# Optimization experiments

Hardware: AMD Instinct MI355X
Metric: run time of the kernel (lower is better)

## Reference

```python
import jax, jax.numpy as jnp
import numpy as np

EMBED_DIM = 1024
NUM_HEADS = 16
HEAD_DIM = EMBED_DIM // NUM_HEADS


def setup_inputs() -> dict:
    key = jax.random.key(0)
    ks = jax.random.split(key, 5)
    B, T, C = 2, 2048, EMBED_DIM
    s_in = 1.0 / np.sqrt(C)
    x = jax.random.normal(ks[0], (B, T, C), dtype=jnp.float32)
    W_qkv = jax.random.normal(ks[1], (C, 3 * C), dtype=jnp.float32) * s_in
    b_qkv = jnp.zeros((3 * C,), dtype=jnp.float32)
    W_out = jax.random.normal(ks[2], (C, C), dtype=jnp.float32) * s_in
    b_out = jnp.zeros((C,), dtype=jnp.float32)
    return {"x": x, "W_qkv": W_qkv, "b_qkv": b_qkv, "W_out": W_out, "b_out": b_out}


def reference(x, W_qkv, b_qkv, W_out, b_out):
    B, T, C = x.shape
    H, D = NUM_HEADS, HEAD_DIM
    qkv = x @ W_qkv + b_qkv                      # [B,T,3C]
    qkv = qkv.reshape(B, T, 3, H, D)
    q = jnp.transpose(qkv[:, :, 0], (0, 2, 1, 3))  # [B,H,T,D]
    k = jnp.transpose(qkv[:, :, 1], (0, 2, 1, 3))
    v = jnp.transpose(qkv[:, :, 2], (0, 2, 1, 3))
    scores = jnp.einsum('bhtd,bhsd->bhts', q, k) / np.sqrt(D).astype(jnp.float32)
    attn = jax.nn.softmax(scores, axis=-1)
    ctx = jnp.einsum('bhts,bhsd->bhtd', attn, v)   # [B,H,T,D]
    ctx = jnp.transpose(ctx, (0, 2, 1, 3)).reshape(B, T, C)
    return ctx @ W_out + b_out
```

## Files before the change

kernel.cpp:

```cpp
#include <hip/hip_runtime.h>
#include <hip/hip_bf16.h>


typedef __attribute__((ext_vector_type(8)))  short short8;
typedef __attribute__((ext_vector_type(4)))  float floatx4;
typedef __attribute__((ext_vector_type(16))) float floatx16;

__device__ inline ushort f2bf(float f) {
    union { __hip_bfloat16 h; ushort u; } c; c.h = __float2bfloat16(f); return c.u;
}

__device__ inline void gld16(const ushort* g, ushort* l) {
    __builtin_amdgcn_global_load_lds(
        (__attribute__((address_space(1))) void*)(g),
        (__attribute__((address_space(3))) void*)(l), 16, 0, 0);
}

__device__ inline void tile_transpose(const float* __restrict__ src, ushort* __restrict__ dst,
                                      int R, int C, int rt, int ct, int t, ushort* L)
{
    const int row = t >> 2, cc = (t & 3) * 16;
    const float* sp = src + (long)(rt * 64 + row) * C + ct * 64 + cc;
    ushort tmp[16];
    #pragma unroll
    for (int i = 0; i < 4; i++) {
        float4 v = *(const float4*)(sp + i * 4);
        tmp[i*4+0]=f2bf(v.x); tmp[i*4+1]=f2bf(v.y); tmp[i*4+2]=f2bf(v.z); tmp[i*4+3]=f2bf(v.w);
    }
    *(uint4*)&L[row * 72 + cc]     = *(uint4*)&tmp[0];
    *(uint4*)&L[row * 72 + cc + 8] = *(uint4*)&tmp[8];
    __syncthreads();
    const int c = t >> 2, rc = (t & 3) * 16;
    ushort o[16];
    #pragma unroll
    for (int j = 0; j < 16; j++) o[j] = L[(rc + j) * 72 + c];
    ushort* dp = dst + (long)(ct * 64 + c) * R + rt * 64 + rc;
    *(uint4*)dp       = *(uint4*)&o[0];
    *(uint4*)(dp + 8) = *(uint4*)&o[8];
}

__global__ __launch_bounds__(256) void prep_kernel(
    const float* __restrict__ x, const float* __restrict__ Wqkv, const float* __restrict__ Wout,
    ushort* __restrict__ xb, ushort* __restrict__ wqkvT, ushort* __restrict__ woutT)
{
    __shared__ __align__(16) ushort L[64 * 72];
    const int bid = blockIdx.x, t = threadIdx.x;
    if (bid < 2048) {
        long i = ((long)bid * 256 + t) * 8;
        float4 a = *(const float4*)(x + i);
        float4 b = *(const float4*)(x + i + 4);
        ushort tmp[8] = { f2bf(a.x), f2bf(a.y), f2bf(a.z), f2bf(a.w),
                          f2bf(b.x), f2bf(b.y), f2bf(b.z), f2bf(b.w) };
        *(uint4*)(xb + i) = *(uint4*)tmp;
    } else if (bid < 2048 + 768) {
        int idx = bid - 2048;
        tile_transpose(Wqkv, wqkvT, 1024, 3072, idx & 15, idx >> 4, t, L);
    } else {
        int idx = bid - 2048 - 768;
        tile_transpose(Wout, woutT, 1024, 1024, idx & 15, idx >> 4, t, L);
    }
}

__global__ __launch_bounds__(256) void qkv_gemm_kernel(
    const ushort* __restrict__ A, const ushort* __restrict__ Bt,
    const float* __restrict__ bias,
    ushort* __restrict__ qbuf, ushort* __restrict__ kbuf, ushort* __restrict__ vtmp)
{
    __shared__ __align__(16) ushort As[2][128 * 32];
    __shared__ __align__(16) ushort Bs[2][128 * 32];

    const int t = threadIdx.x;
    const int w = t >> 6, lane = t & 63;
    const int r = lane & 15, qq = lane >> 4;
    const int wm = w >> 1, wn = w & 1;
    const int rowBase = blockIdx.y * 128, colBase = blockIdx.x * 128;

    const int g_row = lane >> 2, g_kc = (lane & 3) * 8;
    const ushort* aP0 = A  + (long)(rowBase +      w * 16 + g_row) * 1024 + g_kc;
    const ushort* aP1 = A  + (long)(rowBase + 64 + w * 16 + g_row) * 1024 + g_kc;
    const ushort* bP0 = Bt + (long)(colBase +      w * 16 + g_row) * 1024 + g_kc;
    const ushort* bP1 = Bt + (long)(colBase + 64 + w * 16 + g_row) * 1024 + g_kc;

    floatx4 acc[4][4] = {};

    for (int k0 = 0; k0 < 1024; k0 += 64) {
        #pragma unroll
        for (int kk = 0; kk < 2; kk++) {
            gld16(aP0 + k0 + kk * 32, &As[kk][(w * 16) * 32]);
            gld16(aP1 + k0 + kk * 32, &As[kk][(64 + w * 16) * 32]);
            gld16(bP0 + k0 + kk * 32, &Bs[kk][(w * 16) * 32]);
            gld16(bP1 + k0 + kk * 32, &Bs[kk][(64 + w * 16) * 32]);
        }
        __syncthreads();
        #pragma unroll
        for (int kk = 0; kk < 2; kk++) {
            short8 af[4], bf4[4];
            #pragma unroll
            for (int tm = 0; tm < 4; tm++) af[tm]  = *(const short8*)&As[kk][(wm * 64 + tm * 16 + r) * 32 + qq * 8];
            #pragma unroll
            for (int tn = 0; tn < 4; tn++) bf4[tn] = *(const short8*)&Bs[kk][(wn * 64 + tn * 16 + r) * 32 + qq * 8];
            #pragma unroll
            for (int tm = 0; tm < 4; tm++)
                #pragma unroll
                for (int tn = 0; tn < 4; tn++)
                    acc[tm][tn] = __builtin_amdgcn_mfma_f32_16x16x32_bf16(af[tm], bf4[tn], acc[tm][tn], 0, 0, 0);
        }
        __syncthreads();
    }

    #pragma unroll
    for (int tn = 0; tn < 4; tn++) {
        int col = colBase + wn * 64 + tn * 16 + r;
        float bvv = bias[col];
        #pragma unroll
        for (int tm = 0; tm < 4; tm++) {
            #pragma unroll
            for (int reg = 0; reg < 4; reg++) {
                int row = rowBase + wm * 64 + tm * 16 + qq * 4 + reg;
                float val = acc[tm][tn][reg] + bvv;
                if (colBase < 1024)       qbuf[(long)row * 1024 + col]        = f2bf(val);
                else if (colBase < 2048)  kbuf[(long)row * 1024 + col - 1024] = f2bf(val);
                else                      vtmp[(long)row * 1024 + col - 2048] = f2bf(val);
            }
        }
    }
}

__global__ __launch_bounds__(256) void vtrans_kernel(
    const ushort* __restrict__ vsrc, ushort* __restrict__ vt)
{
    __shared__ __align__(16) ushort L[64 * 72];
    const int tt = blockIdx.x, bh = blockIdx.y;
    const int b = bh >> 4, h = bh & 15;
    const int t = threadIdx.x;
    const int row = t >> 2, cc = (t & 3) * 16;
    const ushort* src = vsrc + (long)(b * 2048 + tt * 64 + row) * 1024 + h * 64 + cc;
    *(uint4*)&L[row * 72 + cc]     = *(const uint4*)src;
    *(uint4*)&L[row * 72 + cc + 8] = *(const uint4*)(src + 8);
    __syncthreads();
    const int d = t >> 2, tc = (t & 3) * 16;
    ushort tmp[16];
    #pragma unroll
    for (int j = 0; j < 16; j++) tmp[j] = L[(tc + j) * 72 + d];
    ushort* dst = vt + (long)(bh * 64 + d) * 2048 + tt * 64 + tc;
    *(uint4*)dst       = *(uint4*)&tmp[0];
    *(uint4*)(dst + 8) = *(uint4*)&tmp[8];
}

__global__ __launch_bounds__(256) void out_gemm_kernel(
    const ushort* __restrict__ A, const ushort* __restrict__ Bt,
    const float* __restrict__ bias, float* __restrict__ out)
{
    __shared__ __align__(16) ushort As[2][128 * 32];
    __shared__ __align__(16) ushort Bs[2][64 * 32];

    const int t = threadIdx.x;
    const int w = t >> 6, lane = t & 63;
    const int r = lane & 15, qq = lane >> 4;
    const int wm = w >> 1, wn = w & 1;
    const int rowBase = blockIdx.y * 128, colBase = blockIdx.x * 64;

    const int g_row = lane >> 2, g_kc = (lane & 3) * 8;
    const ushort* aP0 = A  + (long)(rowBase +      w * 16 + g_row) * 1024 + g_kc;
    const ushort* aP1 = A  + (long)(rowBase + 64 + w * 16 + g_row) * 1024 + g_kc;
    const ushort* bP0 = Bt + (long)(colBase +      w * 16 + g_row) * 1024 + g_kc;

    floatx4 acc[4][2] = {};

    for (int k0 = 0; k0 < 1024; k0 += 64) {
        #pragma unroll
        for (int kk = 0; kk < 2; kk++) {
            gld16(aP0 + k0 + kk * 32, &As[kk][(w * 16) * 32]);
            gld16(aP1 + k0 + kk * 32, &As[kk][(64 + w * 16) * 32]);
            gld16(bP0 + k0 + kk * 32, &Bs[kk][(w * 16) * 32]);
        }
        __syncthreads();
        #pragma unroll
        for (int kk = 0; kk < 2; kk++) {
            short8 af[4], bf2[2];
            #pragma unroll
            for (int tm = 0; tm < 4; tm++) af[tm]  = *(const short8*)&As[kk][(wm * 64 + tm * 16 + r) * 32 + qq * 8];
            #pragma unroll
            for (int tn = 0; tn < 2; tn++) bf2[tn] = *(const short8*)&Bs[kk][(wn * 32 + tn * 16 + r) * 32 + qq * 8];
            #pragma unroll
            for (int tm = 0; tm < 4; tm++)
                #pragma unroll
                for (int tn = 0; tn < 2; tn++)
                    acc[tm][tn] = __builtin_amdgcn_mfma_f32_16x16x32_bf16(af[tm], bf2[tn], acc[tm][tn], 0, 0, 0);
        }
        __syncthreads();
    }

    #pragma unroll
    for (int tn = 0; tn < 2; tn++) {
        int col = colBase + wn * 32 + tn * 16 + r;
        float bvv = bias[col];
        #pragma unroll
        for (int tm = 0; tm < 4; tm++) {
            #pragma unroll
            for (int reg = 0; reg < 4; reg++) {
                int row = rowBase + wm * 64 + tm * 16 + qq * 4 + reg;
                out[(long)row * 1024 + col] = acc[tm][tn][reg] + bvv;
            }
        }
    }
}

#define CSCALE 0.18033688011112042f
#define MSHIFT 34.62468098133512f

__global__ __launch_bounds__(256) void attn_kernel(
    ushort* __restrict__ qbuf, const ushort* __restrict__ kbuf,
    const ushort* __restrict__ vt)
{
    __shared__ __align__(16) ushort Ks[64 * 72];
    __shared__ __align__(16) ushort Vs[64 * 72];

    const int t = threadIdx.x;
    const int w = t >> 6, lane = t & 63;
    const int m32 = lane & 31, hi = lane >> 5;

    const int qt = blockIdx.x;
    const int bh = blockIdx.y;
    const int b = bh >> 4, h = bh & 15;
    const long qrow = (long)(b * 2048 + qt * 128 + w * 32 + m32);

    short8 qfrag[4];
    #pragma unroll
    for (int dc = 0; dc < 4; dc++)
        qfrag[dc] = *(const short8*)(qbuf + qrow * 1024 + h * 64 + dc * 16 + hi * 8);

    const int srow = t >> 2, scol = (t & 3) * 16;
    const ushort* kbase = kbuf + (long)(b * 2048) * 1024 + h * 64;
    const ushort* vbase = vt + (long)(bh * 64) * 2048;

    floatx16 o[2] = {};
    float lsum = 0.f;

    for (int kt = 0; kt < 32; kt++) {
        __syncthreads();
        {
            const ushort* kp = kbase + (long)(kt * 64 + srow) * 1024 + scol;
            *(uint4*)&Ks[srow * 72 + scol]     = *(const uint4*)kp;
            *(uint4*)&Ks[srow * 72 + scol + 8] = *(const uint4*)(kp + 8);
            const ushort* vp = vbase + (long)srow * 2048 + kt * 64 + scol;
            *(uint4*)&Vs[srow * 72 + scol]     = *(const uint4*)vp;
            *(uint4*)&Vs[srow * 72 + scol + 8] = *(const uint4*)(vp + 8);
        }
        __syncthreads();

        floatx16 s[2] = {};
        #pragma unroll
        for (int c = 0; c < 2; c++) {
            #pragma unroll
            for (int dc = 0; dc < 4; dc++) {
                short8 kf = *(const short8*)&Ks[(c * 32 + m32) * 72 + dc * 16 + hi * 8];
                s[c] = __builtin_amdgcn_mfma_f32_32x32x16_bf16(kf, qfrag[dc], s[c], 0, 0, 0);
            }
        }

        uint pk[2][8];
        #pragma unroll
        for (int c = 0; c < 2; c++) {
            #pragma unroll
            for (int i = 0; i < 8; i++) {
                float p0 = __builtin_amdgcn_exp2f(s[c][2 * i]     * CSCALE - MSHIFT);
                float p1 = __builtin_amdgcn_exp2f(s[c][2 * i + 1] * CSCALE - MSHIFT);
                lsum += p0 + p1;
                pk[c][i] = (uint)f2bf(p0) | ((uint)f2bf(p1) << 16);
            }
        }

        #pragma unroll
        for (int c = 0; c < 2; c++) {
            #pragma unroll
            for (int kc = 0; kc < 2; kc++) {
                uint s0 = hi ? pk[c][4 * kc + 0] : pk[c][4 * kc + 2];
                uint s1 = hi ? pk[c][4 * kc + 1] : pk[c][4 * kc + 3];
                uint r0 = (uint)__shfl_xor((int)s0, 32);
                uint r1 = (uint)__shfl_xor((int)s1, 32);
                union { uint u[4]; short8 s8; } cv;
                cv.u[0] = hi ? r0 : pk[c][4 * kc + 0];
                cv.u[1] = hi ? r1 : pk[c][4 * kc + 1];
                cv.u[2] = hi ? pk[c][4 * kc + 2] : r0;
                cv.u[3] = hi ? pk[c][4 * kc + 3] : r1;
                #pragma unroll
                for (int dt = 0; dt < 2; dt++) {
                    short8 vf = *(const short8*)&Vs[(dt * 32 + m32) * 72 + c * 32 + kc * 16 + hi * 8];
                    o[dt] = __builtin_amdgcn_mfma_f32_32x32x16_bf16(vf, cv.s8, o[dt], 0, 0, 0);
                }
            }
        }
    }

    lsum += __shfl_xor(lsum, 32);
    float inv = 1.f / lsum;

    #pragma unroll
    for (int dt = 0; dt < 2; dt++) {
        #pragma unroll
        for (int g = 0; g < 4; g++) {
            ushort tmp[4] = { f2bf(o[dt][4*g+0] * inv), f2bf(o[dt][4*g+1] * inv),
                              f2bf(o[dt][4*g+2] * inv), f2bf(o[dt][4*g+3] * inv) };
            *(uint2*)(qbuf + qrow * 1024 + h * 64 + dt * 32 + g * 8 + hi * 4) = *(uint2*)tmp;
        }
    }
}

extern "C" void kernel_launch(void* const* d_in, const int* in_sizes, int n_in,
                              void* d_out, int out_size, void* d_ws, size_t ws_size,
                              hipStream_t stream) {
    const float* x     = (const float*)d_in[0];
    const float* W_qkv = (const float*)d_in[1];
    const float* b_qkv = (const float*)d_in[2];
    const float* W_out = (const float*)d_in[3];
    const float* b_out = (const float*)d_in[4];
    float* out = (float*)d_out;

    ushort* qbuf  = (ushort*)d_ws;
    ushort* kbuf  = qbuf + (size_t)4096 * 1024;
    ushort* vt    = kbuf + (size_t)4096 * 1024;
    ushort* wqkvT = vt + (size_t)2048 * 2048;
    ushort* woutT = wqkvT;

    ushort* xb    = (ushort*)d_out;
    ushort* vtmp  = xb + (size_t)4096 * 1024;

    dim3 blk(256);
    ushort* wqkvT2 = woutT + (size_t)1024 * 1024;

    prep_kernel<<<3072, blk, 0, stream>>>(x, W_qkv, W_out, xb, wqkvT2, woutT);
    qkv_gemm_kernel<<<dim3(24, 32), blk, 0, stream>>>(xb, wqkvT2, b_qkv, qbuf, kbuf, vtmp);
    vtrans_kernel<<<dim3(32, 32), blk, 0, stream>>>(vtmp, vt);
    attn_kernel<<<dim3(16, 32), blk, 0, stream>>>(qbuf, kbuf, vt);
    out_gemm_kernel<<<dim3(16, 32), blk, 0, stream>>>(qbuf, woutT, b_out, out);
}
```

Measured before the change: 207.6 us.

## Prefetch K/V tiles into registers, fold softmax scale into Q, cheaper bf16 pack

The attention kernel now loads the next K/V tile into registers during the current tile's compute and only stores to LDS at the start of each iteration. This hides global load latency and removes one barrier wait on memory. The softmax scale is folded into Q in the QKV GEMM epilogue, dropping a multiply per score, and the bf16 conversion of probabilities uses a simple round-half-up bit trick instead of the library conversion. Workspace pointer naming is also cleaned up. The costs are extra registers and slightly different rounding.

After: 204.2 us. Within noise of the previous version (-1.6%).

```diff
diff --git a/kernel.cpp b/kernel.cpp
--- a/kernel.cpp
+++ b/kernel.cpp
@@ -61,6 +61,8 @@
     }
 }
 
+#define QSCALE 0.18033688011112042f
+
 __global__ __launch_bounds__(256) void qkv_gemm_kernel(
     const ushort* __restrict__ A, const ushort* __restrict__ Bt,
     const float* __restrict__ bias,
@@ -118,7 +120,7 @@
             for (int reg = 0; reg < 4; reg++) {
                 int row = rowBase + wm * 64 + tm * 16 + qq * 4 + reg;
                 float val = acc[tm][tn][reg] + bvv;
-                if (colBase < 1024)       qbuf[(long)row * 1024 + col]        = f2bf(val);
+                if (colBase < 1024)       qbuf[(long)row * 1024 + col]        = f2bf(val * QSCALE);
                 else if (colBase < 2048)  kbuf[(long)row * 1024 + col - 1024] = f2bf(val);
                 else                      vtmp[(long)row * 1024 + col - 2048] = f2bf(val);
             }
@@ -206,7 +208,6 @@
     }
 }
 
-#define CSCALE 0.18033688011112042f
 #define MSHIFT 34.62468098133512f
 
 __global__ __launch_bounds__(256) void attn_kernel(
@@ -237,17 +238,28 @@
     floatx16 o[2] = {};
     float lsum = 0.f;
 
+    uint4 kr0, kr1, vr0, vr1;
+    {
+        const ushort* kp = kbase + (long)srow * 1024 + scol;
+        kr0 = *(const uint4*)kp; kr1 = *(const uint4*)(kp + 8);
+        const ushort* vp = vbase + (long)srow * 2048 + scol;
+        vr0 = *(const uint4*)vp; vr1 = *(const uint4*)(vp + 8);
+    }
+
     for (int kt = 0; kt < 32; kt++) {
         __syncthreads();
-        {
-            const ushort* kp = kbase + (long)(kt * 64 + srow) * 1024 + scol;
-            *(uint4*)&Ks[srow * 72 + scol]     = *(const uint4*)kp;
-            *(uint4*)&Ks[srow * 72 + scol + 8] = *(const uint4*)(kp + 8);
-            const ushort* vp = vbase + (long)srow * 2048 + kt * 64 + scol;
-            *(uint4*)&Vs[srow * 72 + scol]     = *(const uint4*)vp;
-            *(uint4*)&Vs[srow * 72 + scol + 8] = *(const uint4*)(vp + 8);
-        }
-        __syncthreads();
+        *(uint4*)&Ks[srow * 72 + scol]     = kr0;
+        *(uint4*)&Ks[srow * 72 + scol + 8] = kr1;
+        *(uint4*)&Vs[srow * 72 + scol]     = vr0;
+        *(uint4*)&Vs[srow * 72 + scol + 8] = vr1;
+        __syncthreads();
+
+        if (kt < 31) {
+            const ushort* kp = kbase + (long)((kt + 1) * 64 + srow) * 1024 + scol;
+            kr0 = *(const uint4*)kp; kr1 = *(const uint4*)(kp + 8);
+            const ushort* vp = vbase + (long)srow * 2048 + (kt + 1) * 64 + scol;
+            vr0 = *(const uint4*)vp; vr1 = *(const uint4*)(vp + 8);
+        }
 
         floatx16 s[2] = {};
         #pragma unroll
@@ -264,10 +276,12 @@
         for (int c = 0; c < 2; c++) {
             #pragma unroll
             for (int i = 0; i < 8; i++) {
-                float p0 = __builtin_amdgcn_exp2f(s[c][2 * i]     * CSCALE - MSHIFT);
-                float p1 = __builtin_amdgcn_exp2f(s[c][2 * i + 1] * CSCALE - MSHIFT);
+                float p0 = __builtin_amdgcn_exp2f(s[c][2 * i]     - MSHIFT);
+                float p1 = __builtin_amdgcn_exp2f(s[c][2 * i + 1] - MSHIFT);
                 lsum += p0 + p1;
-                pk[c][i] = (uint)f2bf(p0) | ((uint)f2bf(p1) << 16);
+                uint ua = __float_as_uint(p0) + 0x8000u;
+                uint ub = __float_as_uint(p1) + 0x8000u;
+                pk[c][i] = (ua >> 16) | (ub & 0xFFFF0000u);
             }
         }
 
@@ -320,17 +334,15 @@
     ushort* qbuf  = (ushort*)d_ws;
     ushort* kbuf  = qbuf + (size_t)4096 * 1024;
     ushort* vt    = kbuf + (size_t)4096 * 1024;
-    ushort* wqkvT = vt + (size_t)2048 * 2048;
-    ushort* woutT = wqkvT;
+    ushort* woutT = vt + (size_t)2048 * 2048;
+    ushort* wqkvT = woutT + (size_t)1024 * 1024;
 
     ushort* xb    = (ushort*)d_out;
     ushort* vtmp  = xb + (size_t)4096 * 1024;
 
     dim3 blk(256);
-    ushort* wqkvT2 = woutT + (size_t)1024 * 1024;
-
-    prep_kernel<<<3072, blk, 0, stream>>>(x, W_qkv, W_out, xb, wqkvT2, woutT);
-    qkv_gemm_kernel<<<dim3(24, 32), blk, 0, stream>>>(xb, wqkvT2, b_qkv, qbuf, kbuf, vtmp);
+    prep_kernel<<<3072, blk, 0, stream>>>(x, W_qkv, W_out, xb, wqkvT, woutT);
+    qkv_gemm_kernel<<<dim3(24, 32), blk, 0, stream>>>(xb, wqkvT, b_qkv, qbuf, kbuf, vtmp);
     vtrans_kernel<<<dim3(32, 32), blk, 0, stream>>>(vtmp, vt);
     attn_kernel<<<dim3(16, 32), blk, 0, stream>>>(qbuf, kbuf, vt);
     out_gemm_kernel<<<dim3(16, 32), blk, 0, stream>>>(qbuf, woutT, b_out, out);
```
